# Optimization experiments

Measured on AMD Instinct MI355X. Metric: run time of the kernel, lower is better.

The kernel has to match this reference:

```python
import jax, jax.numpy as jnp
import numpy as np

B, T, C, D = 64, 4096, 51, 64
MASK_PROB = 0.3
LN_EPS = 1e-5


def setup_inputs() -> dict:
    key = jax.random.key(0)
    k0, k1, k2, k3, k4 = jax.random.split(key, 5)
    x = jax.random.normal(k0, (B, T, C), dtype=jnp.float32)
    # xavier_uniform_ then *= 0.5 (as in reset_parameters)
    bound = float(np.sqrt(6.0 / (C + D)))
    W = jax.random.uniform(k1, (C, D), jnp.float32, -bound, bound) * 0.5
    Wm = jax.random.uniform(k2, (C, D), jnp.float32, -bound, bound) * 0.5
    gamma = jnp.ones((D,), jnp.float32)
    beta = jnp.zeros((D,), jnp.float32)
    time_mask = jax.random.bernoulli(k3, MASK_PROB, (B, T))
    sensor_mask = jax.random.bernoulli(k4, MASK_PROB, (B, C))
    return {"x": x, "W": W, "Wm": Wm, "gamma": gamma, "beta": beta,
            "time_mask": time_mask, "sensor_mask": sensor_mask}


def reference(x, W, Wm, gamma, beta, time_mask, sensor_mask):
    # mask[b,t,c] = time_mask[b,t] OR sensor_mask[b,c]
    mask = (time_mask[:, :, None] | sensor_mask[:, None, :]).astype(x.dtype)  # [B,T,C]
    # Fused masked reductions (math-equivalent to the broadcast [B,T,C,D] path)
    xu = jnp.einsum('btc,cd->btd', x * (1.0 - mask), W)   # [B,T,D]
    xm = jnp.einsum('btc,cd->btd', mask, Wm)              # [B,T,D]
    out = xu + xm
    # LayerNorm over last dim
    mu = jnp.mean(out, axis=-1, keepdims=True)
    var = jnp.mean((out - mu) ** 2, axis=-1, keepdims=True)
    out = (out - mu) * jax.lax.rsqrt(var + LN_EPS) * gamma + beta
    return out
```

## Files before the change

### kernel.cpp

```cpp
#include <hip/hip_runtime.h>

#define BB 64
#define TT 4096
#define CC 51
#define DD 64
#define LN_EPS 1e-5f

typedef __attribute__((ext_vector_type(8))) short short8;
typedef __attribute__((ext_vector_type(4))) float f32x4;

union FragU { int i[4]; short8 s; };

#define DPP_QP_1032   0xB1
#define DPP_QP_2301   0x4E
#define DPP_ROW_HMIRR 0x141
#define DPP_ROW_MIRR  0x140

__device__ __forceinline__ float dpp_add(float v, int tag) {
  int t;
  switch (tag) {
    case 0: t = __builtin_amdgcn_update_dpp(0, __float_as_int(v), DPP_QP_1032,   0xF, 0xF, true); break;
    case 1: t = __builtin_amdgcn_update_dpp(0, __float_as_int(v), DPP_QP_2301,   0xF, 0xF, true); break;
    case 2: t = __builtin_amdgcn_update_dpp(0, __float_as_int(v), DPP_ROW_HMIRR, 0xF, 0xF, true); break;
    default: t = __builtin_amdgcn_update_dpp(0, __float_as_int(v), DPP_ROW_MIRR, 0xF, 0xF, true); break;
  }
  return v + __int_as_float(t);
}
__device__ __forceinline__ float allsum16(float v) {
  v = dpp_add(v, 0); v = dpp_add(v, 1); v = dpp_add(v, 2); v = dpp_add(v, 3);
  return v;
}
__device__ __forceinline__ float allsum64(float v) {
  v = allsum16(v);
  v += __shfl_xor(v, 16, 64);
  v += __shfl_xor(v, 32, 64);
  return v;
}

__device__ __forceinline__ int pack_hl(float x) {
  const unsigned u = __float_as_uint(x);
  const unsigned h = u >> 16;
  const float hf = __uint_as_float(u & 0xFFFF0000u);
  const unsigned l = __float_as_uint(x - hf) >> 16;
  return (int)(h | (l << 16));
}

__global__ __launch_bounds__(256, 2)
void ipmask_mfma5(const float* __restrict__ x, const float* __restrict__ W,
                  const float* __restrict__ Wm,
                  const float* __restrict__ gamma, const float* __restrict__ beta,
                  const int* __restrict__ tmask, const int* __restrict__ smask,
                  float* __restrict__ out) {
  const int t = threadIdx.x, L = t & 63, w = t >> 6;
  const int q = L >> 4, m16 = L & 15;
  const int gw = (blockIdx.x << 2) + w;
  const int b = gw >> 6;
  const int rowBase = (b << 12) + ((gw & 63) << 6);

  const int* smB = smask + b * CC;

  float xf[4][4][4];
#pragma unroll
  for (int mt = 0; mt < 4; ++mt) {
    const float* xr = x + (size_t)(rowBase + mt * 16 + m16) * CC;
#pragma unroll
    for (int ks = 0; ks < 4; ++ks) {
#pragma unroll
      for (int j = 0; j < 4; ++j) {
        const int c = ks * 16 + q * 4 + j;
        xf[mt][ks][j] = (c < CC) ? xr[c] : 0.0f;
      }
    }
  }
  const int tmv = tmask[rowBase + L];

  __shared__ float red[8][64];
  {
    const int c0 = w * 13, c1 = (c0 + 13 < CC) ? c0 + 13 : CC;
    float bs = 0.0f, f = 0.0f;
    for (int c = c0; c < c1; ++c) {
      const float wmv = Wm[c * DD + L];
      const float sf = (float)smB[c];
      bs = fmaf(sf, wmv, bs);
      f += wmv;
    }
    red[w * 2][L] = bs;
    red[w * 2 + 1][L] = f;
  }
  __syncthreads();
  const float gl = gamma[L], bl = beta[L];
  float biasL, consL;
  {
    const float bs = (red[0][L] + red[2][L]) + (red[4][L] + red[6][L]);
    const float f  = (red[1][L] + red[3][L]) + (red[5][L] + red[7][L]);
    biasL = bs;
    const float s1 = allsum64(f);
    const float s2 = allsum64(f * f);
    const float mu = s1 * (1.0f / 64.0f);
    const float vr = fmaf(-mu, mu, s2 * (1.0f / 64.0f));
    const float rs = rsqrtf(vr + LN_EPS);
    consL = fmaf((f - mu) * rs, gl, bl);
  }
  float bias_[4], cons_[4], g_[4], b_[4];
#pragma unroll
  for (int nt = 0; nt < 4; ++nt) {
    const int src = nt * 16 + m16;
    bias_[nt] = __shfl(biasL, src, 64);
    cons_[nt] = __shfl(consL, src, 64);
    g_[nt]    = __shfl(gl, src, 64);
    b_[nt]    = __shfl(bl, src, 64);
  }

  f32x4 acc[4][4];
#pragma unroll
  for (int nt = 0; nt < 4; ++nt) {
#pragma unroll
    for (int mt = 0; mt < 4; ++mt) {
      acc[mt][nt][0] = bias_[nt]; acc[mt][nt][1] = bias_[nt];
      acc[mt][nt][2] = bias_[nt]; acc[mt][nt][3] = bias_[nt];
    }
  }

#pragma unroll
  for (int ks = 0; ks < 4; ++ks) {
    FragU bmu[4], bcu[4];
#pragma unroll
    for (int j = 0; j < 4; ++j) {
      const int c = ks * 16 + q * 4 + j;
      const int smv = (c < CC) ? smB[c] : 1;
#pragma unroll
      for (int nt = 0; nt < 4; ++nt) {
        const int n = nt * 16 + m16;
        float we = 0.0f;
        if (c < CC) we = W[c * DD + n];
        if (smv) we = 0.0f;
        const unsigned u = __float_as_uint(we);
        const unsigned h = u >> 16;
        const float hf = __uint_as_float(u & 0xFFFF0000u);
        const unsigned l = __float_as_uint(we - hf) >> 16;
        bmu[nt].i[j] = (int)(h | (h << 16));
        bcu[nt].i[j] = (int)l;
      }
    }
#pragma unroll
    for (int mt = 0; mt < 4; ++mt) {
      FragU au;
#pragma unroll
      for (int j = 0; j < 4; ++j) au.i[j] = pack_hl(xf[mt][ks][j]);
#pragma unroll
      for (int nt = 0; nt < 4; ++nt) {
        acc[mt][nt] = __builtin_amdgcn_mfma_f32_16x16x32_bf16(au.s, bmu[nt].s, acc[mt][nt], 0, 0, 0);
        acc[mt][nt] = __builtin_amdgcn_mfma_f32_16x16x32_bf16(au.s, bcu[nt].s, acc[mt][nt], 0, 0, 0);
      }
    }
  }

#pragma unroll
  for (int mt = 0; mt < 4; ++mt) {
#pragma unroll
    for (int rg = 0; rg < 4; ++rg) {
      float su = 0.0f, sq = 0.0f;
#pragma unroll
      for (int nt = 0; nt < 4; ++nt) {
        const float v = acc[mt][nt][rg];
        su += v;
        sq = fmaf(v, v, sq);
      }
      su = allsum16(su);
      sq = allsum16(sq);
      const float mu = su * (1.0f / 64.0f);
      const float vr = fmaf(-mu, mu, sq * (1.0f / 64.0f));
      const float rs = rsqrtf(vr + LN_EPS);
      const int rloc = mt * 16 + q * 4 + rg;
      const int tm = __shfl(tmv, rloc, 64);
      const size_t obase = (size_t)(rowBase + rloc) * DD;
#pragma unroll
      for (int nt = 0; nt < 4; ++nt) {
        float val = fmaf((acc[mt][nt][rg] - mu) * rs, g_[nt], b_[nt]);
        if (tm) val = cons_[nt];
        __builtin_nontemporal_store(val, &out[obase + nt * 16 + m16]);
      }
    }
  }
}

extern "C" void kernel_launch(void* const* d_in, const int* in_sizes, int n_in,
                              void* d_out, int out_size, void* d_ws, size_t ws_size,
                              hipStream_t stream) {
  const float* x     = (const float*)d_in[0];
  const float* W     = (const float*)d_in[1];
  const float* Wm    = (const float*)d_in[2];
  const float* gamma = (const float*)d_in[3];
  const float* beta  = (const float*)d_in[4];
  const int*   tmask = (const int*)d_in[5];
  const int*   smask = (const int*)d_in[6];
  float* out = (float*)d_out;

  ipmask_mfma5<<<dim3(1024), dim3(256), 0, stream>>>(
      x, W, Wm, gamma, beta, tmask, smask, out);
}
```

Before: 126.6 us.

## Replace MFMA split-bf16 GEMM with per-row VALU FMA using scalar-loaded x

Drops the MFMA path, which emulated fp32 with hi/lo bf16 pairs. Each wave now handles 32 rows, with each lane owning one output column and holding the masked W column in registers. Each row's 51 x values come in as wave-uniform scalar loads (s_load) and feed VALU FMAs, then LayerNorm runs as a full-wave reduction. Rows hit by the time mask skip the compute and write the precomputed constant. The grid doubles and occupancy rises, in exchange for a long serial chain of scalar loads with explicit waits, plus dummy vector loads of x that appear to exist only to prefetch the cache.

```diff
diff --git a/kernel.cpp b/kernel.cpp
--- a/kernel.cpp
+++ b/kernel.cpp
@@ -6,10 +6,9 @@
 #define DD 64
 #define LN_EPS 1e-5f
 
-typedef __attribute__((ext_vector_type(8))) short short8;
-typedef __attribute__((ext_vector_type(4))) float f32x4;
-
-union FragU { int i[4]; short8 s; };
+typedef __attribute__((ext_vector_type(16))) int i32x16;
+typedef __attribute__((ext_vector_type(2)))  int i32x2;
+typedef __attribute__((ext_vector_type(4)))  float f32x4;
 
 #define DPP_QP_1032   0xB1
 #define DPP_QP_2301   0x4E
@@ -37,151 +36,142 @@
   return v;
 }
 
-__device__ __forceinline__ int pack_hl(float x) {
-  const unsigned u = __float_as_uint(x);
-  const unsigned h = u >> 16;
-  const float hf = __uint_as_float(u & 0xFFFF0000u);
-  const unsigned l = __float_as_uint(x - hf) >> 16;
-  return (int)(h | (l << 16));
+template <int R>
+__device__ __forceinline__ void doRow(const float* xb, int tm,
+                                      const float (&wq)[CC], float bias,
+                                      float gL, float bL, float cons,
+                                      float* outRow, int L) {
+  if (tm) {
+    __builtin_nontemporal_store(cons, outRow + R * DD + L);
+    return;
+  }
+  i32x16 A, B, C; i32x2 D2; int E;
+  asm volatile(
+      "s_load_dwordx16 %0, %5, %c6\n\t"
+      "s_load_dwordx16 %1, %5, %c7\n\t"
+      "s_load_dwordx16 %2, %5, %c8\n\t"
+      "s_load_dwordx2  %3, %5, %c9\n\t"
+      "s_load_dword    %4, %5, %c10"
+      : "=s"(A), "=s"(B), "=s"(C), "=s"(D2), "=s"(E)
+      : "s"(xb), "i"(R * 204), "i"(R * 204 + 64), "i"(R * 204 + 128),
+        "i"(R * 204 + 192), "i"(R * 204 + 200));
+  asm volatile("s_waitcnt lgkmcnt(0)"
+               : "+s"(A), "+s"(B), "+s"(C), "+s"(D2), "+s"(E));
+  float q0 = bias, q1 = 0.0f, q2 = 0.0f, q3 = 0.0f;
+#define FM(c, S) { const float xs_ = __int_as_float(S);          \
+    if      (((c) & 3) == 0) q0 = fmaf(xs_, wq[c], q0);           \
+    else if (((c) & 3) == 1) q1 = fmaf(xs_, wq[c], q1);           \
+    else if (((c) & 3) == 2) q2 = fmaf(xs_, wq[c], q2);           \
+    else                     q3 = fmaf(xs_, wq[c], q3); }
+  FM(0,A[0])  FM(1,A[1])  FM(2,A[2])  FM(3,A[3])
+  FM(4,A[4])  FM(5,A[5])  FM(6,A[6])  FM(7,A[7])
+  FM(8,A[8])  FM(9,A[9])  FM(10,A[10]) FM(11,A[11])
+  FM(12,A[12]) FM(13,A[13]) FM(14,A[14]) FM(15,A[15])
+  FM(16,B[0])  FM(17,B[1])  FM(18,B[2])  FM(19,B[3])
+  FM(20,B[4])  FM(21,B[5])  FM(22,B[6])  FM(23,B[7])
+  FM(24,B[8])  FM(25,B[9])  FM(26,B[10]) FM(27,B[11])
+  FM(28,B[12]) FM(29,B[13]) FM(30,B[14]) FM(31,B[15])
+  FM(32,C[0])  FM(33,C[1])  FM(34,C[2])  FM(35,C[3])
+  FM(36,C[4])  FM(37,C[5])  FM(38,C[6])  FM(39,C[7])
+  FM(40,C[8])  FM(41,C[9])  FM(42,C[10]) FM(43,C[11])
+  FM(44,C[12]) FM(45,C[13]) FM(46,C[14]) FM(47,C[15])
+  FM(48,D2[0]) FM(49,D2[1]) FM(50,E)
+#undef FM
+  const float o  = (q0 + q1) + (q2 + q3);
+  const float su = allsum64(o);
+  const float sq = allsum64(o * o);
+  const float mu = su * (1.0f / 64.0f);
+  const float vr = fmaf(-mu, mu, sq * (1.0f / 64.0f));
+  const float rs = rsqrtf(vr + LN_EPS);
+  const float val = fmaf((o - mu) * rs, gL, bL);
+  __builtin_nontemporal_store(val, outRow + R * DD + L);
 }
 
-__global__ __launch_bounds__(256, 2)
-void ipmask_mfma5(const float* __restrict__ x, const float* __restrict__ W,
-                  const float* __restrict__ Wm,
-                  const float* __restrict__ gamma, const float* __restrict__ beta,
-                  const int* __restrict__ tmask, const int* __restrict__ smask,
-                  float* __restrict__ out) {
+__global__ __launch_bounds__(256, 4)
+void ipmask_valu(const float* __restrict__ x, const float* __restrict__ W,
+                 const float* __restrict__ Wm,
+                 const float* __restrict__ gamma, const float* __restrict__ beta,
+                 const int* __restrict__ tmask, const int* __restrict__ smask,
+                 float* __restrict__ out) {
   const int t = threadIdx.x, L = t & 63, w = t >> 6;
-  const int q = L >> 4, m16 = L & 15;
-  const int gw = (blockIdx.x << 2) + w;
-  const int b = gw >> 6;
-  const int rowBase = (b << 12) + ((gw & 63) << 6);
+  const int gwU = __builtin_amdgcn_readfirstlane((blockIdx.x << 2) + w);
+  const int rowBase = gwU << 5;
+  const int b = rowBase >> 12;
+  const int* smB = smask + b * CC;
+  const float* xb = x + (size_t)rowBase * CC;
 
-  const int* smB = smask + b * CC;
+  f32x4 p0, p1, p2, p3, p4, p5, p6;
+  const char* xc = (const char*)xb;
+  __builtin_memcpy(&p0, xc + 0 * 1024 + L * 16, 16);
+  __builtin_memcpy(&p1, xc + 1 * 1024 + L * 16, 16);
+  __builtin_memcpy(&p2, xc + 2 * 1024 + L * 16, 16);
+  __builtin_memcpy(&p3, xc + 3 * 1024 + L * 16, 16);
+  __builtin_memcpy(&p4, xc + 4 * 1024 + L * 16, 16);
+  __builtin_memcpy(&p5, xc + 5 * 1024 + L * 16, 16);
+  __builtin_memcpy(&p6, xc + 5504 + L * 16, 16);
 
-  float xf[4][4][4];
+  float wq[CC];
+  float bias = 0.0f, f = 0.0f;
 #pragma unroll
-  for (int mt = 0; mt < 4; ++mt) {
-    const float* xr = x + (size_t)(rowBase + mt * 16 + m16) * CC;
-#pragma unroll
-    for (int ks = 0; ks < 4; ++ks) {
-#pragma unroll
-      for (int j = 0; j < 4; ++j) {
-        const int c = ks * 16 + q * 4 + j;
-        xf[mt][ks][j] = (c < CC) ? xr[c] : 0.0f;
-      }
-    }
+  for (int c = 0; c < CC; ++c) {
+    const float wv  = W[c * DD + L];
+    const float wmv = Wm[c * DD + L];
+    const int   s   = smB[c];
+    wq[c] = s ? 0.0f : wv;
+    bias  = fmaf((float)s, wmv, bias);
+    f += wmv;
   }
-  const int tmv = tmask[rowBase + L];
-
-  __shared__ float red[8][64];
+  const float gL = gamma[L], bL = beta[L];
+  float cons;
   {
-    const int c0 = w * 13, c1 = (c0 + 13 < CC) ? c0 + 13 : CC;
-    float bs = 0.0f, f = 0.0f;
-    for (int c = c0; c < c1; ++c) {
-      const float wmv = Wm[c * DD + L];
-      const float sf = (float)smB[c];
-      bs = fmaf(sf, wmv, bs);
-      f += wmv;
-    }
-    red[w * 2][L] = bs;
-    red[w * 2 + 1][L] = f;
-  }
-  __syncthreads();
-  const float gl = gamma[L], bl = beta[L];
-  float biasL, consL;
-  {
-    const float bs = (red[0][L] + red[2][L]) + (red[4][L] + red[6][L]);
-    const float f  = (red[1][L] + red[3][L]) + (red[5][L] + red[7][L]);
-    biasL = bs;
     const float s1 = allsum64(f);
     const float s2 = allsum64(f * f);
     const float mu = s1 * (1.0f / 64.0f);
     const float vr = fmaf(-mu, mu, s2 * (1.0f / 64.0f));
     const float rs = rsqrtf(vr + LN_EPS);
-    consL = fmaf((f - mu) * rs, gl, bl);
+    cons = fmaf((f - mu) * rs, gL, bL);
   }
-  float bias_[4], cons_[4], g_[4], b_[4];
-#pragma unroll
-  for (int nt = 0; nt < 4; ++nt) {
-    const int src = nt * 16 + m16;
-    bias_[nt] = __shfl(biasL, src, 64);
-    cons_[nt] = __shfl(consL, src, 64);
-    g_[nt]    = __shfl(gl, src, 64);
-    b_[nt]    = __shfl(bl, src, 64);
-  }
+  asm volatile("" :: "v"(p0), "v"(p1), "v"(p2), "v"(p3), "v"(p4), "v"(p5), "v"(p6));
 
-  f32x4 acc[4][4];
-#pragma unroll
-  for (int nt = 0; nt < 4; ++nt) {
-#pragma unroll
-    for (int mt = 0; mt < 4; ++mt) {
-      acc[mt][nt][0] = bias_[nt]; acc[mt][nt][1] = bias_[nt];
-      acc[mt][nt][2] = bias_[nt]; acc[mt][nt][3] = bias_[nt];
-    }
-  }
+  float* outRow = out + (size_t)rowBase * DD;
 
-#pragma unroll
-  for (int ks = 0; ks < 4; ++ks) {
-    FragU bmu[4], bcu[4];
-#pragma unroll
-    for (int j = 0; j < 4; ++j) {
-      const int c = ks * 16 + q * 4 + j;
-      const int smv = (c < CC) ? smB[c] : 1;
-#pragma unroll
-      for (int nt = 0; nt < 4; ++nt) {
-        const int n = nt * 16 + m16;
-        float we = 0.0f;
-        if (c < CC) we = W[c * DD + n];
-        if (smv) we = 0.0f;
-        const unsigned u = __float_as_uint(we);
-        const unsigned h = u >> 16;
-        const float hf = __uint_as_float(u & 0xFFFF0000u);
-        const unsigned l = __float_as_uint(we - hf) >> 16;
-        bmu[nt].i[j] = (int)(h | (h << 16));
-        bcu[nt].i[j] = (int)l;
-      }
-    }
-#pragma unroll
-    for (int mt = 0; mt < 4; ++mt) {
-      FragU au;
-#pragma unroll
-      for (int j = 0; j < 4; ++j) au.i[j] = pack_hl(xf[mt][ks][j]);
-#pragma unroll
-      for (int nt = 0; nt < 4; ++nt) {
-        acc[mt][nt] = __builtin_amdgcn_mfma_f32_16x16x32_bf16(au.s, bmu[nt].s, acc[mt][nt], 0, 0, 0);
-        acc[mt][nt] = __builtin_amdgcn_mfma_f32_16x16x32_bf16(au.s, bcu[nt].s, acc[mt][nt], 0, 0, 0);
-      }
-    }
-  }
-
-#pragma unroll
-  for (int mt = 0; mt < 4; ++mt) {
-#pragma unroll
-    for (int rg = 0; rg < 4; ++rg) {
-      float su = 0.0f, sq = 0.0f;
-#pragma unroll
-      for (int nt = 0; nt < 4; ++nt) {
-        const float v = acc[mt][nt][rg];
-        su += v;
-        sq = fmaf(v, v, sq);
-      }
-      su = allsum16(su);
-      sq = allsum16(sq);
-      const float mu = su * (1.0f / 64.0f);
-      const float vr = fmaf(-mu, mu, sq * (1.0f / 64.0f));
-      const float rs = rsqrtf(vr + LN_EPS);
-      const int rloc = mt * 16 + q * 4 + rg;
-      const int tm = __shfl(tmv, rloc, 64);
-      const size_t obase = (size_t)(rowBase + rloc) * DD;
-#pragma unroll
-      for (int nt = 0; nt < 4; ++nt) {
-        float val = fmaf((acc[mt][nt][rg] - mu) * rs, g_[nt], b_[nt]);
-        if (tm) val = cons_[nt];
-        __builtin_nontemporal_store(val, &out[obase + nt * 16 + m16]);
-      }
-    }
-  }
+  i32x16 tmv;
+  asm volatile("s_load_dwordx16 %0, %1, 0x0\n\ts_waitcnt lgkmcnt(0)"
+               : "=s"(tmv) : "s"(tmask + rowBase));
+  doRow<0>(xb, tmv[0],  wq, bias, gL, bL, cons, outRow, L);
+  doRow<1>(xb, tmv[1],  wq, bias, gL, bL, cons, outRow, L);
+  doRow<2>(xb, tmv[2],  wq, bias, gL, bL, cons, outRow, L);
+  doRow<3>(xb, tmv[3],  wq, bias, gL, bL, cons, outRow, L);
+  doRow<4>(xb, tmv[4],  wq, bias, gL, bL, cons, outRow, L);
+  doRow<5>(xb, tmv[5],  wq, bias, gL, bL, cons, outRow, L);
+  doRow<6>(xb, tmv[6],  wq, bias, gL, bL, cons, outRow, L);
+  doRow<7>(xb, tmv[7],  wq, bias, gL, bL, cons, outRow, L);
+  doRow<8>(xb, tmv[8],  wq, bias, gL, bL, cons, outRow, L);
+  doRow<9>(xb, tmv[9],  wq, bias, gL, bL, cons, outRow, L);
+  doRow<10>(xb, tmv[10], wq, bias, gL, bL, cons, outRow, L);
+  doRow<11>(xb, tmv[11], wq, bias, gL, bL, cons, outRow, L);
+  doRow<12>(xb, tmv[12], wq, bias, gL, bL, cons, outRow, L);
+  doRow<13>(xb, tmv[13], wq, bias, gL, bL, cons, outRow, L);
+  doRow<14>(xb, tmv[14], wq, bias, gL, bL, cons, outRow, L);
+  doRow<15>(xb, tmv[15], wq, bias, gL, bL, cons, outRow, L);
+  asm volatile("s_load_dwordx16 %0, %1, 0x40\n\ts_waitcnt lgkmcnt(0)"
+               : "=s"(tmv) : "s"(tmask + rowBase));
+  doRow<16>(xb, tmv[0],  wq, bias, gL, bL, cons, outRow, L);
+  doRow<17>(xb, tmv[1],  wq, bias, gL, bL, cons, outRow, L);
+  doRow<18>(xb, tmv[2],  wq, bias, gL, bL, cons, outRow, L);
+  doRow<19>(xb, tmv[3],  wq, bias, gL, bL, cons, outRow, L);
+  doRow<20>(xb, tmv[4],  wq, bias, gL, bL, cons, outRow, L);
+  doRow<21>(xb, tmv[5],  wq, bias, gL, bL, cons, outRow, L);
+  doRow<22>(xb, tmv[6],  wq, bias, gL, bL, cons, outRow, L);
+  doRow<23>(xb, tmv[7],  wq, bias, gL, bL, cons, outRow, L);
+  doRow<24>(xb, tmv[8],  wq, bias, gL, bL, cons, outRow, L);
+  doRow<25>(xb, tmv[9],  wq, bias, gL, bL, cons, outRow, L);
+  doRow<26>(xb, tmv[10], wq, bias, gL, bL, cons, outRow, L);
+  doRow<27>(xb, tmv[11], wq, bias, gL, bL, cons, outRow, L);
+  doRow<28>(xb, tmv[12], wq, bias, gL, bL, cons, outRow, L);
+  doRow<29>(xb, tmv[13], wq, bias, gL, bL, cons, outRow, L);
+  doRow<30>(xb, tmv[14], wq, bias, gL, bL, cons, outRow, L);
+  doRow<31>(xb, tmv[15], wq, bias, gL, bL, cons, outRow, L);
 }
 
 extern "C" void kernel_launch(void* const* d_in, const int* in_sizes, int n_in,
@@ -196,6 +186,6 @@
   const int*   smask = (const int*)d_in[6];
   float* out = (float*)d_out;
 
-  ipmask_mfma5<<<dim3(1024), dim3(256), 0, stream>>>(
+  ipmask_valu<<<dim3(2048), dim3(256), 0, stream>>>(
       x, W, Wm, gamma, beta, tmask, smask, out);
 }
```

New measurement: 144.1 us. 1.14x slower.
